# Kernel optimization log

Measured on AMD Instinct MI355X. Metric: run time of the kernel, lower is better.

Reference implementation:

```python
import jax, jax.numpy as jnp
import numpy as np

B, CQ, CKV, E = 8, 256, 256, 256
H, W = 64, 64
HP, WP = 32, 32


def setup_inputs() -> dict:
    key = jax.random.key(0)
    ks = jax.random.split(key, 6)
    C = jax.random.normal(ks[0], (B, CQ, H, W), dtype=jnp.float32)
    P = jax.random.normal(ks[1], (B, CKV, HP, WP), dtype=jnp.float32)
    # 1x1 conv weights, kaiming-ish scale; stored as [out_ch, in_ch]
    theta_w = jax.random.normal(ks[2], (E, CQ), dtype=jnp.float32) * (1.0 / np.sqrt(CQ))
    phi_w = jax.random.normal(ks[3], (E, CKV), dtype=jnp.float32) * (1.0 / np.sqrt(CKV))
    g_w = jax.random.normal(ks[4], (E, CKV), dtype=jnp.float32) * (1.0 / np.sqrt(CKV))
    out_w = jax.random.normal(ks[5], (CQ, E), dtype=jnp.float32) * (1.0 / np.sqrt(E))
    return {"C": C, "P": P, "theta_w": theta_w, "phi_w": phi_w, "g_w": g_w, "out_w": out_w}


def reference(C, P, theta_w, phi_w, g_w, out_w):
    b, _, h, w = C.shape
    e = theta_w.shape[0]
    # 1x1 convs are channel GEMMs
    theta_C = jnp.einsum('bchw,ec->behw', C, theta_w).reshape(b, e, h * w)   # [B,E,Nq]
    phi_P = jnp.einsum('bchw,ec->behw', P, phi_w).reshape(b, e, -1)          # [B,E,Nkv]
    g_P = jnp.einsum('bchw,ec->behw', P, g_w).reshape(b, e, -1)              # [B,E,Nkv]
    attn = jnp.einsum('ben,bem->bnm', theta_C, phi_P) / (e ** 0.5)           # [B,Nq,Nkv]
    attn = jax.nn.softmax(attn, axis=-1)
    out = jnp.einsum('bem,bnm->ben', g_P, attn).reshape(b, e, h, w)          # [B,E,H,W]
    out = jnp.einsum('behw,ce->bchw', out, out_w)                            # [B,CQ,H,W]
    return jnp.concatenate([C, out], axis=1)
```

## Files before the change

kernel.cpp:

```cpp
#include <hip/hip_runtime.h>


typedef __attribute__((ext_vector_type(8))) short short8;
typedef __attribute__((ext_vector_type(16))) float f32x16;
typedef unsigned short ushort_t;

__device__ __forceinline__ unsigned short f2bf(float f) {
    unsigned int u = __float_as_uint(f);
    u += 0x7FFFu + ((u >> 16) & 1u);
    return (unsigned short)(u >> 16);
}
__device__ __forceinline__ unsigned int pack2bf(float a, float b) {
    return (unsigned int)f2bf(a) | ((unsigned int)f2bf(b) << 16);
}
__device__ __forceinline__ void gload16(const ushort_t* g, ushort_t* l) {
    __builtin_amdgcn_global_load_lds(
        (const __attribute__((address_space(1))) unsigned int*)g,
        (__attribute__((address_space(3))) unsigned int*)l, 16, 0, 0);
}
__device__ __forceinline__ f32x16 zero16() {
    f32x16 z;
#pragma unroll
    for (int i = 0; i < 16; ++i) z[i] = 0.f;
    return z;
}

__global__ __launch_bounds__(256) void prep_w(const float* __restrict__ thw,
                                              const float* __restrict__ phw,
                                              const float* __restrict__ ow,
                                              const float* __restrict__ gw,
                                              ushort_t* __restrict__ thc,
                                              ushort_t* __restrict__ phc,
                                              ushort_t* __restrict__ w2c) {
    int blk = blockIdx.x;
    int t = threadIdx.x;
    if (blk < 512) {
        int which = blk >> 8;
        int e = blk & 255, c = t;
        const float* src = which ? phw : thw;
        ushort_t* dst = which ? phc : thc;
        int idx = ((((e >> 5) * 16 + (c >> 4)) * 64 + ((c >> 3) & 1) * 32 + (e & 31)) << 3) + (c & 7);
        dst[idx] = f2bf(src[e * 256 + c]);
    } else {
        int c0 = (blk - 512) * 8;
        float acc[8] = {};
        for (int e = 0; e < 256; ++e) {
            float g = gw[e * 256 + t];
#pragma unroll
            for (int i = 0; i < 8; ++i) acc[i] += ow[(c0 + i) * 256 + e] * g;
        }
#pragma unroll
        for (int i = 0; i < 8; ++i) {
            int c = c0 + i, k = t;
            int idx = ((((c >> 5) * 16 + (k >> 4)) * 64 + ((k >> 3) & 1) * 32 + (c & 31)) << 3) + (k & 7);
            w2c[idx] = f2bf(acc[i]);
        }
    }
}

__global__ __launch_bounds__(256, 2) void proj_all(const ushort_t* __restrict__ thc,
                                                   const ushort_t* __restrict__ phc,
                                                   const ushort_t* __restrict__ w2c,
                                                   const float* __restrict__ C,
                                                   const float* __restrict__ P,
                                                   ushort_t* __restrict__ thetaA,
                                                   ushort_t* __restrict__ phiA,
                                                   ushort_t* __restrict__ gVx) {
    __shared__ float Xs[256][68];
    int blk = blockIdx.x;
    int tid = threadIdx.x, lane = tid & 63, wid = tid >> 6;
    int l31 = lane & 31, lh = lane >> 5;
    const int wq = wid & 1, we = wid >> 1;

    int role, b, nt, N;
    const ushort_t* Wc;
    const float* Xg;
    ushort_t* outp;
    float scale = 1.f;
    if (blk < 512) {
        role = 0; b = blk & 7; nt = blk >> 3;
        Wc = thc; Xg = C + (size_t)b * 1048576; outp = thetaA + (size_t)b * 1048576;
        N = 4096; scale = 1.4426950408889634f / 16.0f;
    } else if (blk < 640) {
        int r = blk - 512; role = 1; b = r & 7; nt = r >> 3;
        Wc = phc; Xg = P + (size_t)b * 262144; outp = phiA + (size_t)b * 262144;
        N = 1024;
    } else {
        int r = blk - 640; role = 2; b = r & 7; nt = r >> 3;
        Wc = w2c; Xg = P + (size_t)b * 262144; outp = gVx + (size_t)b * 262144;
        N = 1024;
    }

    {
        const float* Xb = Xg + nt * 64;
#pragma unroll
        for (int i = 0; i < 16; ++i) {
            int idx = i * 256 + tid;
            int row = idx >> 4, c4 = (idx & 15) * 4;
            *(float4*)&Xs[row][c4] = *(const float4*)(Xb + (size_t)row * N + c4);
        }
    }
    __syncthreads();

    const int n0 = nt * 64 + wq * 32;
    const int ncr = (n0 >> 5) * 16;
    const int q = wq * 32 + l31;

    f32x16 o[4];
#pragma unroll
    for (int f = 0; f < 4; ++f) o[f] = zero16();

#pragma unroll
    for (int ks = 0; ks < 16; ++ks) {
        const int cb = ks * 16 + lh * 8;
        union PW { unsigned int u[4]; short8 v; } xw;
#pragma unroll
        for (int j = 0; j < 4; ++j)
            xw.u[j] = pack2bf(Xs[cb + 2 * j][q], Xs[cb + 2 * j + 1][q]);
#pragma unroll
        for (int f2 = 0; f2 < 4; ++f2) {
            int f = we * 4 + f2;
            short8 wf = *(const short8*)(Wc + ((size_t)(f * 16 + ks) * 64 + lane) * 8);
            o[f2] = __builtin_amdgcn_mfma_f32_32x32x16_bf16(wf, xw.v, o[f2], 0, 0, 0);
        }
    }

    if (role < 2) {
#pragma unroll
        for (int f2 = 0; f2 < 4; ++f2) {
            int f = we * 4 + f2;
#pragma unroll
            for (int rq = 0; rq < 4; ++rq) {
                uint2 st;
                st.x = pack2bf(o[f2][4 * rq + 0] * scale, o[f2][4 * rq + 1] * scale);
                st.y = pack2bf(o[f2][4 * rq + 2] * scale, o[f2][4 * rq + 3] * scale);
                size_t addr = ((size_t)(ncr + f * 2 + (rq >> 1)) * 64 + l31 + 32 * (rq & 1)) * 8 + 4 * lh;
                *(uint2*)(outp + addr) = st;
            }
        }
    } else {
        int kvq = (n0 >> 4) + (l31 >> 4);
        int lhw = 32 * ((l31 >> 3) & 1);
        int kl = l31 & 7;
#pragma unroll
        for (int f2 = 0; f2 < 4; ++f2) {
            int f = we * 4 + f2;
#pragma unroll
            for (int r2 = 0; r2 < 16; ++r2) {
                int crow = (r2 & 3) + 8 * (r2 >> 2) + 4 * lh;
                size_t addr = ((size_t)(f * 64 + kvq) * 64 + crow + lhw) * 8 + kl;
                outp[addr] = f2bf(o[f2][r2]);
            }
        }
    }
}

__global__ __launch_bounds__(512, 2) void attn7(const ushort_t* __restrict__ thetaA,
                                                const ushort_t* __restrict__ phiA,
                                                const ushort_t* __restrict__ gVx,
                                                const float* __restrict__ Cf,
                                                float* __restrict__ out) {
    const int b = blockIdx.x & 7, qt = blockIdx.x >> 3;
    const int tid = threadIdx.x, lane = tid & 63, wid = tid >> 6;
    const int l31 = lane & 31, lh = lane >> 5;
    const int h = wid >> 2, qg = wid & 3;

    __shared__ __align__(16) ushort_t smem[65536];
    __shared__ float rlS[4][32];

    const ushort_t* thA = thetaA + (size_t)b * 1048576;
    const ushort_t* phA = phiA + (size_t)b * 262144;
    const ushort_t* gVb = gVx + (size_t)b * 262144;

    auto stageK = [&](int j) {
        if ((wid & 2) == 0) {
            int hh = wid >> 2;
            const ushort_t* src = phA + (size_t)(2 * j + hh) * 8192 + (wid & 1) * 4096 + lane * 8;
            ushort_t* dst = smem + hh * 16384 + (j & 1) * 8192 + (wid & 1) * 4096;
#pragma unroll
            for (int i = 0; i < 8; ++i) gload16(src + i * 512, dst + i * 512);
        }
    };
    auto stageV = [&](int j) {
        if ((wid & 2) == 2) {
            int hh = wid >> 2;
#pragma unroll
            for (int cg2 = 0; cg2 < 4; ++cg2) {
                int cg = (wid & 1) * 4 + cg2;
#pragma unroll
                for (int jj = 0; jj < 2; ++jj) {
                    const ushort_t* src =
                        gVb + ((size_t)(cg * 64 + 4 * j + 2 * hh + jj) * 64 + lane) * 8;
                    ushort_t* dst = smem + 32768 + hh * 16384 + (j & 1) * 8192 + cg * 1024 + jj * 512;
                    gload16(src, dst);
                }
            }
        }
    };

    stageK(0); stageK(1); stageV(0);

    short8 qf[16];
    {
        const int qcr = (qt * 4 + qg) * 16;
#pragma unroll
        for (int ks = 0; ks < 16; ++ks)
            qf[ks] = *(const short8*)(thA + ((size_t)(qcr + ks) * 64 + lane) * 8);
    }

    f32x16 o[8];
#pragma unroll
    for (int f = 0; f < 8; ++f) o[f] = zero16();
    float rl = 0.f;

    const size_t cbase = (size_t)b * 1048576 + (size_t)qt * 128 + (size_t)l31 * 4;
    const size_t dofs = (size_t)b * 1048576;
    size_t cpo = 0;
    float4 cpv;

    asm volatile("s_waitcnt vmcnt(0)" ::: "memory");
    __builtin_amdgcn_s_barrier();
    __builtin_amdgcn_sched_barrier(0);

    f32x16 s = zero16();
    {
        const ushort_t* Kb = smem + h * 16384;
#pragma unroll
        for (int ks = 0; ks < 16; ++ks) {
            short8 kf = *(const short8*)(Kb + (size_t)ks * 512 + lane * 8);
            s = __builtin_amdgcn_mfma_f32_32x32x16_bf16(kf, qf[ks], s, 0, 0, 0);
        }
    }

    for (int it = 0; it < 16; ++it) {
        asm volatile("s_waitcnt vmcnt(0)" ::: "memory");
        __builtin_amdgcn_s_barrier();
        __builtin_amdgcn_sched_barrier(0);
        if (it < 14) stageK(it + 2);
        if (it < 15) stageV(it + 1);

        if (it > 0) *(float4*)(out + cpo + dofs) = cpv;
        cpo = cbase + (size_t)(it * 16 + 2 * wid + lh) * 4096;
        cpv = *(const float4*)(Cf + cpo);

        float ps = 0.f;
#pragma unroll
        for (int r = 0; r < 16; ++r) {
            s[r] = __builtin_amdgcn_exp2f(s[r]);
            ps += s[r];
        }
        ps += __shfl_xor(ps, 32);
        rl += ps;

        unsigned int a0 = pack2bf(s[0], s[1]),   b0 = pack2bf(s[4], s[5]);
        unsigned int a1 = pack2bf(s[2], s[3]),   b1 = pack2bf(s[6], s[7]);
        unsigned int a2 = pack2bf(s[8], s[9]),   b2 = pack2bf(s[12], s[13]);
        unsigned int a3 = pack2bf(s[10], s[11]), b3 = pack2bf(s[14], s[15]);
        asm volatile("v_permlane32_swap_b32 %0, %1" : "+v"(a0), "+v"(b0));
        asm volatile("v_permlane32_swap_b32 %0, %1" : "+v"(a1), "+v"(b1));
        asm volatile("v_permlane32_swap_b32 %0, %1" : "+v"(a2), "+v"(b2));
        asm volatile("v_permlane32_swap_b32 %0, %1" : "+v"(a3), "+v"(b3));
        union PW { unsigned int u[4]; short8 v; };
        PW p0; p0.u[0] = a0; p0.u[1] = a1; p0.u[2] = b0; p0.u[3] = b1;
        PW p1; p1.u[0] = a2; p1.u[1] = a3; p1.u[2] = b2; p1.u[3] = b3;

        const ushort_t* Vb = smem + 32768 + h * 16384 + (it & 1) * 8192;
        const ushort_t* Kb = smem + h * 16384 + ((it + 1) & 1) * 8192;
        __builtin_amdgcn_s_setprio(1);
        if (it < 15) {
            f32x16 sn = zero16();
#pragma unroll
            for (int ks2 = 0; ks2 < 2; ++ks2) {
                short8 pf = ks2 ? p1.v : p0.v;
#pragma unroll
                for (int f = 0; f < 8; ++f) {
                    short8 vf = *(const short8*)(Vb + (size_t)f * 1024 + ks2 * 512 + lane * 8);
                    o[f] = __builtin_amdgcn_mfma_f32_32x32x16_bf16(vf, pf, o[f], 0, 0, 0);
                    int ks = ks2 * 8 + f;
                    short8 kf = *(const short8*)(Kb + (size_t)ks * 512 + lane * 8);
                    sn = __builtin_amdgcn_mfma_f32_32x32x16_bf16(kf, qf[ks], sn, 0, 0, 0);
                }
            }
            s = sn;
        } else {
#pragma unroll
            for (int ks2 = 0; ks2 < 2; ++ks2) {
                short8 pf = ks2 ? p1.v : p0.v;
#pragma unroll
                for (int f = 0; f < 8; ++f) {
                    short8 vf = *(const short8*)(Vb + (size_t)f * 1024 + ks2 * 512 + lane * 8);
                    o[f] = __builtin_amdgcn_mfma_f32_32x32x16_bf16(vf, pf, o[f], 0, 0, 0);
                }
            }
        }
        __builtin_amdgcn_s_setprio(0);
        __builtin_amdgcn_sched_barrier(0);
    }

    *(float4*)(out + cpo + dofs) = cpv;

    __syncthreads();

    if (wid >= 4) {
        float* part = (float*)smem + (size_t)(wid - 4) * 8192;
#pragma unroll
        for (int f = 0; f < 8; ++f)
#pragma unroll
            for (int r = 0; r < 16; ++r) {
                int e = f * 32 + (r & 3) + 8 * (r >> 2) + 4 * lh;
                part[e * 32 + l31] = o[f][r];
            }
        if (lane < 32) rlS[wid - 4][l31] = rl;
    }
    __syncthreads();
    if (wid < 4) {
        float inv = 1.f / (rl + rlS[wid][l31]);
        const float* part = (const float*)smem + (size_t)wid * 8192;
        float* ob = out + (size_t)b * 2097152 + (size_t)256 * 4096 + qt * 128 + qg * 32 + l31;
#pragma unroll
        for (int f = 0; f < 8; ++f)
#pragma unroll
            for (int r = 0; r < 16; ++r) {
                int e = f * 32 + (r & 3) + 8 * (r >> 2) + 4 * lh;
                ob[(size_t)e * 4096] = (o[f][r] + part[e * 32 + l31]) * inv;
            }
    }
}


extern "C" void kernel_launch(void* const* d_in, const int* in_sizes, int n_in,
                              void* d_out, int out_size, void* d_ws, size_t ws_size,
                              hipStream_t stream) {
    const float* C       = (const float*)d_in[0];
    const float* P       = (const float*)d_in[1];
    const float* theta_w = (const float*)d_in[2];
    const float* phi_w   = (const float*)d_in[3];
    const float* g_w     = (const float*)d_in[4];
    const float* out_w   = (const float*)d_in[5];
    float* out = (float*)d_out;

    ushort_t* ws = (ushort_t*)d_ws;
    ushort_t* thetaA = ws;
    ushort_t* phiA   = ws + 8388608;
    ushort_t* gVx    = ws + 10485760;
    ushort_t* thWc   = ws + 12582912;
    ushort_t* phWc   = ws + 12648448;
    ushort_t* w2c    = ws + 12713984;

    prep_w<<<544, 256, 0, stream>>>(theta_w, phi_w, out_w, g_w, thWc, phWc, w2c);
    proj_all<<<768, 256, 0, stream>>>(thWc, phWc, w2c, C, P, thetaA, phiA, gVx);
    attn7<<<256, 512, 0, stream>>>(thetaA, phiA, gVx, C, out);
}
```

Before: 111.6 us.

## Split attention work by output channel halves instead of KV halves

The attention kernel's eight waves no longer split the key/value sequence into two halves. Each wave now computes the full score tile for its query group over all keys, and the PV product covers only its half of the embedding channels. This drops the cross-wave shared-memory reduction of partial outputs and row sums at the end, and the software-pipelined overlap of the next score GEMM with the current PV GEMM. In exchange, QK^T work is computed twice (once per channel-half wave pair), and there is less overlap between the score and PV phases.

```diff
diff --git a/kernel.cpp b/kernel.cpp
--- a/kernel.cpp
+++ b/kernel.cpp
@@ -155,7 +155,7 @@
     }
 }
 
-__global__ __launch_bounds__(512, 2) void attn7(const ushort_t* __restrict__ thetaA,
+__global__ __launch_bounds__(512, 2) void attn9(const ushort_t* __restrict__ thetaA,
                                                 const ushort_t* __restrict__ phiA,
                                                 const ushort_t* __restrict__ gVx,
                                                 const float* __restrict__ Cf,
@@ -163,54 +163,48 @@
     const int b = blockIdx.x & 7, qt = blockIdx.x >> 3;
     const int tid = threadIdx.x, lane = tid & 63, wid = tid >> 6;
     const int l31 = lane & 31, lh = lane >> 5;
-    const int h = wid >> 2, qg = wid & 3;
+    const int g = wid & 3, eh = wid >> 2;
 
     __shared__ __align__(16) ushort_t smem[65536];
-    __shared__ float rlS[4][32];
 
     const ushort_t* thA = thetaA + (size_t)b * 1048576;
     const ushort_t* phA = phiA + (size_t)b * 262144;
     const ushort_t* gVb = gVx + (size_t)b * 262144;
 
-    auto stageK = [&](int j) {
-        if ((wid & 2) == 0) {
-            int hh = wid >> 2;
-            const ushort_t* src = phA + (size_t)(2 * j + hh) * 8192 + (wid & 1) * 4096 + lane * 8;
-            ushort_t* dst = smem + hh * 16384 + (j & 1) * 8192 + (wid & 1) * 4096;
+    auto stage = [&](int j, int d) {
+        if (wid < 4) {
+            const ushort_t* src = phA + (size_t)j * 16384 + (size_t)wid * 4096 + lane * 8;
+            ushort_t* dst = smem + d * 16384 + wid * 4096;
 #pragma unroll
             for (int i = 0; i < 8; ++i) gload16(src + i * 512, dst + i * 512);
-        }
-    };
-    auto stageV = [&](int j) {
-        if ((wid & 2) == 2) {
-            int hh = wid >> 2;
-#pragma unroll
-            for (int cg2 = 0; cg2 < 4; ++cg2) {
-                int cg = (wid & 1) * 4 + cg2;
-#pragma unroll
-                for (int jj = 0; jj < 2; ++jj) {
-                    const ushort_t* src =
-                        gVb + ((size_t)(cg * 64 + 4 * j + 2 * hh + jj) * 64 + lane) * 8;
-                    ushort_t* dst = smem + 32768 + hh * 16384 + (j & 1) * 8192 + cg * 1024 + jj * 512;
+        } else {
+            int w = wid - 4;
+#pragma unroll
+            for (int q2 = 0; q2 < 2; ++q2) {
+                int f = w * 2 + q2;
+#pragma unroll
+                for (int jj = 0; jj < 4; ++jj) {
+                    const ushort_t* src = gVb + ((size_t)(f * 64 + j * 4 + jj) * 64 + lane) * 8;
+                    ushort_t* dst = smem + 32768 + d * 16384 + f * 2048 + jj * 512;
                     gload16(src, dst);
                 }
             }
         }
     };
 
-    stageK(0); stageK(1); stageV(0);
+    stage(0, 0);
 
     short8 qf[16];
     {
-        const int qcr = (qt * 4 + qg) * 16;
+        const int qcr = (qt * 4 + g) * 16;
 #pragma unroll
         for (int ks = 0; ks < 16; ++ks)
             qf[ks] = *(const short8*)(thA + ((size_t)(qcr + ks) * 64 + lane) * 8);
     }
 
-    f32x16 o[8];
-#pragma unroll
-    for (int f = 0; f < 8; ++f) o[f] = zero16();
+    f32x16 o[4];
+#pragma unroll
+    for (int f = 0; f < 4; ++f) o[f] = zero16();
     float rl = 0.f;
 
     const size_t cbase = (size_t)b * 1048576 + (size_t)qt * 128 + (size_t)l31 * 4;
@@ -218,112 +212,85 @@
     size_t cpo = 0;
     float4 cpv;
 
-    asm volatile("s_waitcnt vmcnt(0)" ::: "memory");
-    __builtin_amdgcn_s_barrier();
-    __builtin_amdgcn_sched_barrier(0);
-
-    f32x16 s = zero16();
-    {
-        const ushort_t* Kb = smem + h * 16384;
-#pragma unroll
-        for (int ks = 0; ks < 16; ++ks) {
-            short8 kf = *(const short8*)(Kb + (size_t)ks * 512 + lane * 8);
-            s = __builtin_amdgcn_mfma_f32_32x32x16_bf16(kf, qf[ks], s, 0, 0, 0);
-        }
-    }
-
     for (int it = 0; it < 16; ++it) {
         asm volatile("s_waitcnt vmcnt(0)" ::: "memory");
         __builtin_amdgcn_s_barrier();
         __builtin_amdgcn_sched_barrier(0);
-        if (it < 14) stageK(it + 2);
-        if (it < 15) stageV(it + 1);
+        if (it < 15) stage(it + 1, (it + 1) & 1);
 
         if (it > 0) *(float4*)(out + cpo + dofs) = cpv;
         cpo = cbase + (size_t)(it * 16 + 2 * wid + lh) * 4096;
         cpv = *(const float4*)(Cf + cpo);
 
+        const ushort_t* Kb = smem + (it & 1) * 16384;
+        const ushort_t* Vb = smem + 32768 + (it & 1) * 16384 + eh * 8192;
+
+        f32x16 s0 = zero16(), s1 = zero16();
+#pragma unroll
+        for (int ks = 0; ks < 16; ++ks) {
+            short8 kf0 = *(const short8*)(Kb + (size_t)ks * 512 + lane * 8);
+            short8 kf1 = *(const short8*)(Kb + 8192 + (size_t)ks * 512 + lane * 8);
+            s0 = __builtin_amdgcn_mfma_f32_32x32x16_bf16(kf0, qf[ks], s0, 0, 0, 0);
+            s1 = __builtin_amdgcn_mfma_f32_32x32x16_bf16(kf1, qf[ks], s1, 0, 0, 0);
+        }
+
         float ps = 0.f;
 #pragma unroll
         for (int r = 0; r < 16; ++r) {
-            s[r] = __builtin_amdgcn_exp2f(s[r]);
-            ps += s[r];
+            s0[r] = __builtin_amdgcn_exp2f(s0[r]);
+            s1[r] = __builtin_amdgcn_exp2f(s1[r]);
+            ps += s0[r] + s1[r];
         }
         ps += __shfl_xor(ps, 32);
         rl += ps;
 
-        unsigned int a0 = pack2bf(s[0], s[1]),   b0 = pack2bf(s[4], s[5]);
-        unsigned int a1 = pack2bf(s[2], s[3]),   b1 = pack2bf(s[6], s[7]);
-        unsigned int a2 = pack2bf(s[8], s[9]),   b2 = pack2bf(s[12], s[13]);
-        unsigned int a3 = pack2bf(s[10], s[11]), b3 = pack2bf(s[14], s[15]);
+        unsigned int a0 = pack2bf(s0[0], s0[1]),   b0 = pack2bf(s0[4], s0[5]);
+        unsigned int a1 = pack2bf(s0[2], s0[3]),   b1 = pack2bf(s0[6], s0[7]);
+        unsigned int a2 = pack2bf(s0[8], s0[9]),   b2 = pack2bf(s0[12], s0[13]);
+        unsigned int a3 = pack2bf(s0[10], s0[11]), b3 = pack2bf(s0[14], s0[15]);
         asm volatile("v_permlane32_swap_b32 %0, %1" : "+v"(a0), "+v"(b0));
         asm volatile("v_permlane32_swap_b32 %0, %1" : "+v"(a1), "+v"(b1));
         asm volatile("v_permlane32_swap_b32 %0, %1" : "+v"(a2), "+v"(b2));
         asm volatile("v_permlane32_swap_b32 %0, %1" : "+v"(a3), "+v"(b3));
+        unsigned int c0 = pack2bf(s1[0], s1[1]),   d0 = pack2bf(s1[4], s1[5]);
+        unsigned int c1 = pack2bf(s1[2], s1[3]),   d1 = pack2bf(s1[6], s1[7]);
+        unsigned int c2 = pack2bf(s1[8], s1[9]),   d2 = pack2bf(s1[12], s1[13]);
+        unsigned int c3 = pack2bf(s1[10], s1[11]), d3 = pack2bf(s1[14], s1[15]);
+        asm volatile("v_permlane32_swap_b32 %0, %1" : "+v"(c0), "+v"(d0));
+        asm volatile("v_permlane32_swap_b32 %0, %1" : "+v"(c1), "+v"(d1));
+        asm volatile("v_permlane32_swap_b32 %0, %1" : "+v"(c2), "+v"(d2));
+        asm volatile("v_permlane32_swap_b32 %0, %1" : "+v"(c3), "+v"(d3));
         union PW { unsigned int u[4]; short8 v; };
-        PW p0; p0.u[0] = a0; p0.u[1] = a1; p0.u[2] = b0; p0.u[3] = b1;
-        PW p1; p1.u[0] = a2; p1.u[1] = a3; p1.u[2] = b2; p1.u[3] = b3;
-
-        const ushort_t* Vb = smem + 32768 + h * 16384 + (it & 1) * 8192;
-        const ushort_t* Kb = smem + h * 16384 + ((it + 1) & 1) * 8192;
+        PW pw[4];
+        pw[0].u[0] = a0; pw[0].u[1] = a1; pw[0].u[2] = b0; pw[0].u[3] = b1;
+        pw[1].u[0] = a2; pw[1].u[1] = a3; pw[1].u[2] = b2; pw[1].u[3] = b3;
+        pw[2].u[0] = c0; pw[2].u[1] = c1; pw[2].u[2] = d0; pw[2].u[3] = d1;
+        pw[3].u[0] = c2; pw[3].u[1] = c3; pw[3].u[2] = d2; pw[3].u[3] = d3;
+
         __builtin_amdgcn_s_setprio(1);
-        if (it < 15) {
-            f32x16 sn = zero16();
-#pragma unroll
-            for (int ks2 = 0; ks2 < 2; ++ks2) {
-                short8 pf = ks2 ? p1.v : p0.v;
-#pragma unroll
-                for (int f = 0; f < 8; ++f) {
-                    short8 vf = *(const short8*)(Vb + (size_t)f * 1024 + ks2 * 512 + lane * 8);
-                    o[f] = __builtin_amdgcn_mfma_f32_32x32x16_bf16(vf, pf, o[f], 0, 0, 0);
-                    int ks = ks2 * 8 + f;
-                    short8 kf = *(const short8*)(Kb + (size_t)ks * 512 + lane * 8);
-                    sn = __builtin_amdgcn_mfma_f32_32x32x16_bf16(kf, qf[ks], sn, 0, 0, 0);
-                }
+#pragma unroll
+        for (int ks2 = 0; ks2 < 4; ++ks2) {
+            short8 pf = pw[ks2].v;
+#pragma unroll
+            for (int fl = 0; fl < 4; ++fl) {
+                short8 vf = *(const short8*)(Vb + (size_t)fl * 2048 + ks2 * 512 + lane * 8);
+                o[fl] = __builtin_amdgcn_mfma_f32_32x32x16_bf16(vf, pf, o[fl], 0, 0, 0);
             }
-            s = sn;
-        } else {
-#pragma unroll
-            for (int ks2 = 0; ks2 < 2; ++ks2) {
-                short8 pf = ks2 ? p1.v : p0.v;
-#pragma unroll
-                for (int f = 0; f < 8; ++f) {
-                    short8 vf = *(const short8*)(Vb + (size_t)f * 1024 + ks2 * 512 + lane * 8);
-                    o[f] = __builtin_amdgcn_mfma_f32_32x32x16_bf16(vf, pf, o[f], 0, 0, 0);
-                }
-            }
         }
         __builtin_amdgcn_s_setprio(0);
-        __builtin_amdgcn_sched_barrier(0);
     }
 
     *(float4*)(out + cpo + dofs) = cpv;
 
-    __syncthreads();
-
-    if (wid >= 4) {
-        float* part = (float*)smem + (size_t)(wid - 4) * 8192;
-#pragma unroll
-        for (int f = 0; f < 8; ++f)
-#pragma unroll
-            for (int r = 0; r < 16; ++r) {
-                int e = f * 32 + (r & 3) + 8 * (r >> 2) + 4 * lh;
-                part[e * 32 + l31] = o[f][r];
-            }
-        if (lane < 32) rlS[wid - 4][l31] = rl;
-    }
-    __syncthreads();
-    if (wid < 4) {
-        float inv = 1.f / (rl + rlS[wid][l31]);
-        const float* part = (const float*)smem + (size_t)wid * 8192;
-        float* ob = out + (size_t)b * 2097152 + (size_t)256 * 4096 + qt * 128 + qg * 32 + l31;
-#pragma unroll
-        for (int f = 0; f < 8; ++f)
-#pragma unroll
-            for (int r = 0; r < 16; ++r) {
-                int e = f * 32 + (r & 3) + 8 * (r >> 2) + 4 * lh;
-                ob[(size_t)e * 4096] = (o[f][r] + part[e * 32 + l31]) * inv;
-            }
+    float inv = 1.f / rl;
+    float* ob = out + (size_t)b * 2097152 + (size_t)256 * 4096 + qt * 128 + g * 32 + l31;
+#pragma unroll
+    for (int fl = 0; fl < 4; ++fl) {
+#pragma unroll
+        for (int r = 0; r < 16; ++r) {
+            int e = eh * 128 + fl * 32 + (r & 3) + 8 * (r >> 2) + 4 * lh;
+            ob[(size_t)e * 4096] = o[fl][r] * inv;
+        }
     }
 }
 
@@ -349,5 +316,5 @@
 
     prep_w<<<544, 256, 0, stream>>>(theta_w, phi_w, out_w, g_w, thWc, phWc, w2c);
     proj_all<<<768, 256, 0, stream>>>(thWc, phWc, w2c, C, P, thetaA, phiA, gVx);
-    attn7<<<256, 512, 0, stream>>>(thetaA, phiA, gVx, C, out);
-}
+    attn9<<<256, 512, 0, stream>>>(thetaA, phiA, gVx, C, out);
+}
```

Result: slower. 123.3 us (+10.5%).
